# Performance work log

Measured on AMD Instinct MI355X. Metric: run time of the kernel, lower is better.

## Reference

```python
import jax, jax.numpy as jnp
import numpy as np

EPS = 1e-5  # RMSNorm epsilon


def rmsnorm(x, w):
    return x * jax.lax.rsqrt(jnp.mean(x * x, axis=-1, keepdims=True) + EPS) * w


def mamba_forward(u, in_proj_w, conv_w, conv_b, x_proj_w, dt_proj_w, dt_proj_b,
                  A_log, D_param, mamba_out_w):
    # u: (b, L, dm) -- canonical Mamba block (expand=2, d_state=16, d_conv=4)
    b, L, dm = u.shape
    di, ds = A_log.shape
    dtr = dt_proj_w.shape[1]
    xz = jnp.einsum('bld,ed->ble', u, in_proj_w)          # (b,L,2*di)
    x_, z = jnp.split(xz, 2, axis=-1)                     # each (b,L,di)
    # causal depthwise conv over the sequence axis
    dconv = conv_w.shape[-1]
    xc = jnp.transpose(x_, (0, 2, 1))                     # (b,di,L)
    xc = jnp.pad(xc, ((0, 0), (0, 0), (dconv - 1, 0)))
    xc = jax.lax.conv_general_dilated(xc, conv_w, window_strides=(1,), padding='VALID',
                                      dimension_numbers=('NCH', 'OIH', 'NCH'),
                                      feature_group_count=di)
    xc = xc + conv_b[None, :, None]
    x_ = jax.nn.silu(jnp.transpose(xc, (0, 2, 1)))        # (b,L,di)
    # input-dependent dt, B, C
    x_dbl = jnp.einsum('bld,ed->ble', x_, x_proj_w)       # (b,L,dtr+2*ds)
    dt, B, C = jnp.split(x_dbl, [dtr, dtr + ds], axis=-1)
    delta = jax.nn.softplus(jnp.einsum('blr,dr->bld', dt, dt_proj_w) + dt_proj_b)  # (b,L,di)
    A = -jnp.exp(A_log)                                   # (di,ds)

    def step(h, inp):
        d_t, B_t, C_t, x_t = inp                          # (b,di),(b,ds),(b,ds),(b,di)
        dA = jnp.exp(d_t[:, :, None] * A)                 # (b,di,ds)
        h = dA * h + (d_t * x_t)[:, :, None] * B_t[:, None, :]
        y = jnp.einsum('bds,bs->bd', h, C_t)
        return h, y

    xs = (jnp.moveaxis(delta, 1, 0), jnp.moveaxis(B, 1, 0),
          jnp.moveaxis(C, 1, 0), jnp.moveaxis(x_, 1, 0))
    h0 = jnp.zeros((b, di, ds), dtype=u.dtype)
    _, ys = jax.lax.scan(step, h0, xs)                    # ys: (L,b,di)
    y = jnp.moveaxis(ys, 0, 1) + x_ * D_param             # (b,L,di)
    y = y * jax.nn.silu(z)
    return jnp.einsum('bld,od->blo', y, mamba_out_w)      # (b,L,dm)


def conv1x1(W, bvec, t):
    # t: (b, cin, L) -> (b, cout, L)
    return jnp.einsum('oi,bit->bot', W, t) + bvec[None, :, None]


def reference(x, w_norm1, w_norm2, W_ip, b_ip, W_fp, b_fp, W_wp, b_wp, W_op, b_op,
              in_proj_w, conv_w, conv_b, x_proj_w, dt_proj_w, dt_proj_b,
              A_log, D_param, mamba_out_w):
    # x: (b, L, D) -- module's (b, c, l) with l == input_dim = D, c == seq = L
    residual = x
    xn = rmsnorm(x, w_norm1)                 # RMSNorm over last (input_dim) axis
    xt = jnp.transpose(xn, (0, 2, 1))        # 'b c l -> b l c' : (b, D, L)
    ssm = conv1x1(W_ip, b_ip, xt)            # (b, 2D, L)
    ssm = conv1x1(W_fp, b_fp, ssm)           # (b, 2D, L)
    u = jnp.transpose(ssm, (0, 2, 1))        # (b, L, 2D): seq=L, d_model=2D
    m = mamba_forward(u, in_proj_w, conv_w, conv_b, x_proj_w, dt_proj_w, dt_proj_b,
                      A_log, D_param, mamba_out_w)
    m = rmsnorm(m, w_norm2) + u              # PostNormMamba residual
    ssm = jnp.transpose(m, (0, 2, 1))        # (b, 2D, L)
    w = conv1x1(W_wp, b_wp, xt)              # (b, 2D, L)
    w = w * jax.nn.sigmoid(w)                # swish
    out = conv1x1(W_op, b_op, w * ssm)       # (b, D, L)
    return jnp.transpose(out, (0, 2, 1)) + residual


def setup_inputs():
    key = jax.random.key(0)
    ks = jax.random.split(key, 16)
    D, L, b = 64, 4096, 4
    dm, di, ds, dconv = 2 * D, 4 * D, 16, 4
    dtr = (dm + 15) // 16  # dt_rank = ceil(d_model/16) = 8

    def n(k, shape, fan_in):
        return jax.random.normal(k, shape, jnp.float32) * (1.0 / np.sqrt(fan_in))

    return {
        'x': jax.random.normal(ks[0], (b, L, D), jnp.float32),
        'w_norm1': jnp.ones((D,), jnp.float32),
        'w_norm2': jnp.ones((dm,), jnp.float32),
        'W_ip': n(ks[1], (2 * D, D), D), 'b_ip': jnp.zeros((2 * D,), jnp.float32),
        'W_fp': n(ks[2], (2 * D, 2 * D), 2 * D), 'b_fp': jnp.zeros((2 * D,), jnp.float32),
        'W_wp': n(ks[3], (2 * D, D), D), 'b_wp': jnp.zeros((2 * D,), jnp.float32),
        'W_op': n(ks[4], (D, 2 * D), 2 * D), 'b_op': jnp.zeros((D,), jnp.float32),
        'in_proj_w': n(ks[5], (2 * di, dm), dm),
        'conv_w': n(ks[6], (di, 1, dconv), dconv),
        'conv_b': jnp.zeros((di,), jnp.float32),
        'x_proj_w': n(ks[7], (dtr + 2 * ds, di), di),
        'dt_proj_w': n(ks[8], (di, dtr), dtr),
        'dt_proj_b': jnp.full((di,), float(np.log(np.expm1(0.01))), jnp.float32),
        'A_log': jnp.log(jnp.broadcast_to(jnp.arange(1, ds + 1, dtype=jnp.float32), (di, ds))),
        'D_param': jnp.ones((di,), jnp.float32),
        'mamba_out_w': n(ks[9], (dm, di), di),
    }
```

## Files before the change

kernel.cpp:

```cpp
#include <hip/hip_runtime.h>
#include <hip/hip_bf16.h>

typedef __hip_bfloat16 bf16;
typedef __attribute__((ext_vector_type(8))) short bf16x8;
typedef __attribute__((ext_vector_type(4))) float f32x4;
#define DEV __device__ __forceinline__

constexpr int SEQ  = 4096;
constexpr int NB   = 4;
constexpr int NTOK = NB * SEQ;
constexpr float EPS = 1e-5f;
constexpr int NCH = 32;
constexpr int NCHUNK = SEQ / NCH;
constexpr float LOG2E = 1.44269504f;

constexpr int OFF_WDT  = 0;
constexpr int OFF_WB   = 2048;
constexpr int WB_IP = 0;
constexpr int WB_WP = 8192;
constexpr int WB_FP = 16384;
constexpr int WB_PR = 32768;
constexpr int WB_MO = 98304;
constexpr int WB_OP = 131072;
constexpr int WB_XP = 139264;
constexpr int WB_TOT = 151552;
constexpr int OFF_XDBL = OFF_WB + WB_TOT / 2;
constexpr int OFF_R1   = OFF_XDBL + NTOK * 40;
constexpr int OFF_WSW  = OFF_R1   + 1048576;
constexpr int OFF_U    = OFF_WSW  + 1048576;
constexpr int OFF_R2   = OFF_U    + 1048576;
constexpr int OFF_SILUZ= OFF_R2   + 2097152;
constexpr int OFF_XC   = OFF_SILUZ+ 2097152;
constexpr int OFF_G    = OFF_XC   + 2097152;
constexpr int OFF_FLAG = OFF_G    + 2097152;
constexpr int OFF_SUMM = OFF_FLAG + 16;
constexpr int OFF_HIN  = OFF_SUMM + 64 * NCHUNK * 256 * 2;

DEV float b2f(bf16 x) { return __bfloat162float(x); }
DEV bf16 f2b(float x) { return __float2bfloat16(x); }
DEV short shof(bf16 h) { short s; __builtin_memcpy(&s, &h, 2); return s; }
DEV float ldin(const void* p, int i, int f) {
  return f ? ((const float*)p)[i] : b2f(((const bf16*)p)[i]);
}
DEV unsigned pack2(float a, float b) {
  bf16 ha = f2b(a), hb = f2b(b);
  unsigned short ua, ub;
  __builtin_memcpy(&ua, &ha, 2); __builtin_memcpy(&ub, &hb, 2);
  return (unsigned)ua | ((unsigned)ub << 16);
}
DEV float lo16f(unsigned u) { return __int_as_float((int)(u << 16)); }
DEV float hi16f(unsigned u) { return __int_as_float((int)(u & 0xffff0000u)); }
template<int CTRL>
DEV float dpp_add(float v) {
  int r = __builtin_amdgcn_update_dpp(0, __float_as_int(v), CTRL, 0xF, 0xF, false);
  return v + __int_as_float(r);
}
DEV float exp2f_fast(float a) { return __builtin_amdgcn_exp2f(a); }
DEV float softplus(float a) {
  return (a > 20.f) ? a : __logf(1.f + exp2f_fast(a * LOG2E));
}
DEV float silu(float a) { return a / (1.f + __expf(-a)); }

DEV void cpw(int e, int base, int count, const void* __restrict__ src,
             bf16* __restrict__ wb, int f) {
  int r = e - base;
  if (r >= 0 && r < count) wb[base + r] = f2b(ldin(src, r, f));
}
__global__ __launch_bounds__(256) void prep_k(
    const void* __restrict__ w_ip, const void* __restrict__ w_wp, const void* __restrict__ w_fp,
    const void* __restrict__ w_pr, const void* __restrict__ w_mo, const void* __restrict__ w_op,
    const void* __restrict__ w_x,  const void* __restrict__ w_dt,
    const void* __restrict__ x, float* __restrict__ wsf, int* __restrict__ flagp)
{
  __shared__ int cnt;
  if (threadIdx.x == 0) cnt = 0;
  __syncthreads();
  {
    float v = b2f(((const bf16*)x)[threadIdx.x]);
    int ok = (v == v) && fabsf(v) > 1e-4f && fabsf(v) < 100.f;
    atomicAdd(&cnt, ok);
  }
  __syncthreads();
  int f = (cnt > 204) ? 0 : 1;
  if (blockIdx.x == 0 && threadIdx.x == 0) *flagp = f;

  int e = blockIdx.x * 256 + threadIdx.x;
  bf16* wb = (bf16*)(wsf + OFF_WB);
  cpw(e, WB_IP, 8192,  w_ip, wb, f);
  cpw(e, WB_WP, 8192,  w_wp, wb, f);
  cpw(e, WB_FP, 16384, w_fp, wb, f);
  cpw(e, WB_PR, 65536, w_pr, wb, f);
  cpw(e, WB_MO, 32768, w_mo, wb, f);
  cpw(e, WB_OP, 8192,  w_op, wb, f);
  {
    int r = e - WB_XP;
    if (r >= 0 && r < 12288) wb[WB_XP + r] = (r < 10240) ? f2b(ldin(w_x, r, f)) : f2b(0.f);
  }
  if (e < 2048) {
    int r = e >> 8, d = e & 255;
    wsf[OFF_WDT + e] = ldin(w_dt, d * 8 + r, f);
  }
}

__global__ __launch_bounds__(512) void fm_k(
    const void* __restrict__ x, const void* __restrict__ w1, const float* __restrict__ wsf,
    const void* __restrict__ b_ip, const void* __restrict__ b_wp, const void* __restrict__ b_fp,
    bf16* __restrict__ wsw, bf16* __restrict__ u, bf16* __restrict__ xpre,
    bf16* __restrict__ siluz, const int* __restrict__ flagp)
{
  __shared__ __align__(16) char smem[33280];
  short* xn   = (short*)smem;
  short* t1   = (short*)(smem + 4608);
  short* ul   = (short*)(smem + 13312);
  short* wswl = (short*)(smem + 22016);
  short* xzl  = (short*)smem;

  const int f = *flagp;
  const int tid = threadIdx.x;
  const int tok0 = blockIdx.x * 32;
  {
    const int token = tid >> 4, r = tid & 15;
    float v[4]; float ss = 0.f;
    #pragma unroll
    for (int k = 0; k < 4; ++k) {
      v[k] = ldin(x, (tok0 + token) * 64 + r * 4 + k, f);
      ss += v[k] * v[k];
    }
    ss += __shfl_xor(ss, 1, 16); ss += __shfl_xor(ss, 2, 16);
    ss += __shfl_xor(ss, 4, 16); ss += __shfl_xor(ss, 8, 16);
    float sc = rsqrtf(ss * (1.f / 64.f) + EPS);
    unsigned* dst = (unsigned*)xn + token * 36 + r * 2;
    #pragma unroll
    for (int k = 0; k < 2; ++k) {
      int i = r * 4 + k * 2;
      dst[k] = pack2(v[k*2] * sc * ldin(w1, i, f), v[k*2+1] * sc * ldin(w1, i + 1, f));
    }
  }
  __syncthreads();
  const int lane = tid & 63, m = lane & 15, q = lane >> 4;
  const int w = tid >> 6;
  {
    const int wt = w >> 2, ng = w & 3;
    const bf16* W = (const bf16*)(wsf + OFF_WB) + (wt ? WB_WP : WB_IP);
    const void* bia = wt ? b_wp : b_ip;
    bf16x8 a[2][2];
    #pragma unroll
    for (int mt = 0; mt < 2; ++mt)
      #pragma unroll
      for (int kk = 0; kk < 2; ++kk)
        a[mt][kk] = *(const bf16x8*)&xn[(mt * 16 + m) * 72 + kk * 32 + q * 8];
    #pragma unroll
    for (int nti = 0; nti < 2; ++nti) {
      int nt = ng * 2 + nti;
      int n = nt * 16 + m;
      f32x4 acc[2] = {{0,0,0,0},{0,0,0,0}};
      #pragma unroll
      for (int kk = 0; kk < 2; ++kk) {
        bf16x8 b = *(const bf16x8*)(W + (nt * 16 + m) * 64 + kk * 32 + q * 8);
        #pragma unroll
        for (int mt = 0; mt < 2; ++mt)
          acc[mt] = __builtin_amdgcn_mfma_f32_16x16x32_bf16(a[mt][kk], b, acc[mt], 0, 0, 0);
      }
      float bv = ldin(bia, n, f);
      #pragma unroll
      for (int mt = 0; mt < 2; ++mt)
        #pragma unroll
        for (int r = 0; r < 4; ++r) {
          float v = acc[mt][r] + bv;
          int row = mt * 16 + q * 4 + r;
          if (wt) wswl[row * 128 + n] = shof(f2b(silu(v)));
          else    t1[row * 136 + n] = shof(f2b(v));
        }
    }
  }
  __syncthreads();
  {
    int row = tid >> 4, c8 = (tid & 15) * 8;
    uint4 v = *(const uint4*)&wswl[row * 128 + c8];
    *(uint4*)(wsw + (tok0 + row) * 128 + c8) = v;
  }
  {
    const bf16* WF = (const bf16*)(wsf + OFF_WB) + WB_FP;
    bf16x8 a[2][4];
    #pragma unroll
    for (int mt = 0; mt < 2; ++mt)
      #pragma unroll
      for (int kk = 0; kk < 4; ++kk)
        a[mt][kk] = *(const bf16x8*)&t1[(mt * 16 + m) * 136 + kk * 32 + q * 8];
    {
      int nt = w;
      int n = nt * 16 + m;
      f32x4 acc[2] = {{0,0,0,0},{0,0,0,0}};
      #pragma unroll
      for (int kk = 0; kk < 4; ++kk) {
        bf16x8 b = *(const bf16x8*)(WF + (nt * 16 + m) * 128 + kk * 32 + q * 8);
        #pragma unroll
        for (int mt = 0; mt < 2; ++mt)
          acc[mt] = __builtin_amdgcn_mfma_f32_16x16x32_bf16(a[mt][kk], b, acc[mt], 0, 0, 0);
      }
      float bv = ldin(b_fp, n, f);
      #pragma unroll
      for (int mt = 0; mt < 2; ++mt)
        #pragma unroll
        for (int r = 0; r < 4; ++r)
          ul[(mt * 16 + q * 4 + r) * 136 + n] = shof(f2b(acc[mt][r] + bv));
    }
  }
  __syncthreads();
  {
    int row = tid >> 4, c8 = (tid & 15) * 8;
    uint4 v = *(const uint4*)&ul[row * 136 + c8];
    *(uint4*)(u + (tok0 + row) * 128 + c8) = v;
  }
  {
    const bf16* WP = (const bf16*)(wsf + OFF_WB) + WB_PR;
    bf16x8 a[2][4];
    #pragma unroll
    for (int mt = 0; mt < 2; ++mt)
      #pragma unroll
      for (int kk = 0; kk < 4; ++kk)
        a[mt][kk] = *(const bf16x8*)&ul[(mt * 16 + m) * 136 + kk * 32 + q * 8];
    __syncthreads();
    #pragma unroll
    for (int nti = 0; nti < 4; ++nti) {
      int nt = w * 4 + nti;
      int n = nt * 16 + m;
      f32x4 acc[2] = {{0,0,0,0},{0,0,0,0}};
      #pragma unroll
      for (int kk = 0; kk < 4; ++kk) {
        bf16x8 b = *(const bf16x8*)(WP + (nt * 16 + m) * 128 + kk * 32 + q * 8);
        #pragma unroll
        for (int mt = 0; mt < 2; ++mt)
          acc[mt] = __builtin_amdgcn_mfma_f32_16x16x32_bf16(a[mt][kk], b, acc[mt], 0, 0, 0);
      }
      #pragma unroll
      for (int mt = 0; mt < 2; ++mt)
        #pragma unroll
        for (int r = 0; r < 4; ++r) {
          int row = mt * 16 + q * 4 + r;
          float v = acc[mt][r];
          xzl[row * 520 + n] = shof(f2b(n < 256 ? v : silu(v)));
        }
    }
  }
  __syncthreads();
  {
    #pragma unroll
    for (int k = 0; k < 4; ++k) {
      int chunk = tid + k * 512;
      int row = chunk >> 6, seg = chunk & 63;
      uint4 v = *(const uint4*)&xzl[row * 520 + seg * 8];
      int n0 = seg * 8;
      if (n0 < 256) *(uint4*)(xpre + (tok0 + row) * 256 + n0) = v;
      else          *(uint4*)(siluz + (tok0 + row) * 256 + (n0 - 256)) = v;
    }
  }
}

__global__ __launch_bounds__(256) void conv_k(
    const bf16* __restrict__ xpre, const void* __restrict__ cw, const void* __restrict__ cb,
    const float* __restrict__ wsf, bf16* __restrict__ xc, float* __restrict__ xdbl,
    const int* __restrict__ flagp)
{
  __shared__ short xh[35 * 256];
  __shared__ short cs[32 * 264];
  const int f = *flagp;
  const int tid = threadIdx.x;
  const int tok0 = blockIdx.x * 32;
  const bool seqstart = (tok0 & (SEQ - 1)) == 0;
  for (int c = tid; c < 1120; c += 256) {
    int e0 = c * 8;
    int tt = e0 >> 8, i = e0 & 255;
    int gtok = tok0 + tt - 3;
    uint4* dst = (uint4*)(xh + e0);
    if (gtok >= 0 && !(seqstart && tt < 3)) *dst = *(const uint4*)(xpre + gtok * 256 + i);
    else                                    *dst = make_uint4(0, 0, 0, 0);
  }
  __syncthreads();
  {
    const int ch0 = (tid & 63) * 4;
    const int t0 = (tid >> 6) * 8;
    float w4[4][4], cb4[4];
    #pragma unroll
    for (int c = 0; c < 4; ++c) {
      cb4[c] = ldin(cb, ch0 + c, f);
      #pragma unroll
      for (int k = 0; k < 4; ++k) w4[c][k] = ldin(cw, (ch0 + c) * 4 + k, f);
    }
    float win[11][4];
    #pragma unroll
    for (int r = 0; r < 11; ++r) {
      uint2 v = *(const uint2*)&xh[(t0 + r) * 256 + ch0];
      win[r][0] = lo16f(v.x); win[r][1] = hi16f(v.x);
      win[r][2] = lo16f(v.y); win[r][3] = hi16f(v.y);
    }
    #pragma unroll
    for (int t = 0; t < 8; ++t) {
      unsigned pk[2];
      #pragma unroll
      for (int cp = 0; cp < 2; ++cp) {
        float o[2];
        #pragma unroll
        for (int ci = 0; ci < 2; ++ci) {
          int c = cp * 2 + ci;
          float acc = cb4[c];
          #pragma unroll
          for (int k = 0; k < 4; ++k) acc = fmaf(win[t + k][c], w4[c][k], acc);
          o[ci] = silu(acc);
        }
        pk[cp] = pack2(o[0], o[1]);
      }
      uint2 pv = make_uint2(pk[0], pk[1]);
      *(uint2*)&cs[(t0 + t) * 264 + ch0] = pv;
      *(uint2*)(xc + (tok0 + t0 + t) * 256 + ch0) = pv;
    }
  }
  __syncthreads();
  const int w = tid >> 6;
  if (w < 2) {
    const bf16* Wx = (const bf16*)(wsf + OFF_WB) + WB_XP;
    const int lane = tid & 63, m = lane & 15, quad = lane >> 4;
    f32x4 acc[3] = {{0,0,0,0},{0,0,0,0},{0,0,0,0}};
    #pragma unroll
    for (int k0 = 0; k0 < 256; k0 += 32) {
      bf16x8 af = *(const bf16x8*)&cs[(w * 16 + m) * 264 + k0 + quad * 8];
      #pragma unroll
      for (int nt = 0; nt < 3; ++nt) {
        bf16x8 bfr = *(const bf16x8*)(Wx + (nt * 16 + m) * 256 + k0 + quad * 8);
        acc[nt] = __builtin_amdgcn_mfma_f32_16x16x32_bf16(af, bfr, acc[nt], 0, 0, 0);
      }
    }
    #pragma unroll
    for (int nt = 0; nt < 3; ++nt) {
      int n = nt * 16 + m;
      if (n < 40) {
        #pragma unroll
        for (int r = 0; r < 4; ++r)
          xdbl[(tok0 + w * 16 + quad * 4 + r) * 40 + n] = acc[nt][r];
      }
    }
  }
}

__global__ __launch_bounds__(256) void scanF_k(
    const float* __restrict__ xdbl, const bf16* __restrict__ xc,
    const void* __restrict__ A_log, const void* __restrict__ dt_b,
    const float* __restrict__ WDT, float* __restrict__ summ, const int* __restrict__ flagp)
{
  const int f = *flagp;
  const int tid = threadIdx.x;
  const int bb = blockIdx.x >> 2, dgsup = blockIdx.x & 3, c = blockIdx.y;
  const int dgsub = tid >> 6, lane = tid & 63, dl = lane >> 2, squad = lane & 3;
  const int dg = dgsup * 4 + dgsub;
  const int bxOld = bb * 16 + dg;
  const int d_comp = dg * 16 + dl;
  const int bd = tid & 63;
  const int d_stg = dgsup * 64 + bd;
  const int bdc = dgsub * 16 + dl;
  const int tok_base = bb * SEQ + c * NCH;

  __shared__ float dt_l[NCH * 8];
  __shared__ float dx_l[16 * 64 * 2];
  __shared__ float Bp[16 * 16];

  float Aval2[4];
  #pragma unroll
  for (int j = 0; j < 4; ++j)
    Aval2[j] = -__expf(ldin(A_log, d_comp * 16 + squad * 4 + j, f)) * LOG2E;
  const float dtb_stg = ldin(dt_b, d_stg, f);
  float wdt[8];
  #pragma unroll
  for (int r = 0; r < 8; ++r) wdt[r] = WDT[r * 256 + d_stg];

  float h[4] = {0.f, 0.f, 0.f, 0.f};
  float sdlt = 0.f;

  if (tid < 64)
    *(float4*)(dt_l + tid * 4) = *(const float4*)(xdbl + (tok_base + (tid >> 1)) * 40 + (tid & 1) * 4);

  #pragma unroll 1
  for (int half = 0; half < 2; ++half) {
    const int tb = half * 16;
    __syncthreads();
    {
      int tl = tid >> 4, s = tid & 15;
      Bp[tid] = xdbl[(tok_base + tb + tl) * 40 + 8 + s];
    }
    #pragma unroll
    for (int k = 0; k < 4; ++k) {
      int tl = (tid >> 6) + k * 4;
      int tok = tok_base + tb + tl;
      const float* dtr = dt_l + (tb + tl) * 8;
      float a = dtb_stg;
      #pragma unroll
      for (int r = 0; r < 8; ++r) a = fmaf(dtr[r], wdt[r], a);
      float dlt = softplus(a);
      float xcv = b2f(xc[tok * 256 + d_stg]);
      *(float2*)(dx_l + (tl * 64 + bd) * 2) = make_float2(dlt, dlt * xcv);
    }
    __syncthreads();

    #pragma unroll 8
    for (int tl = 0; tl < 16; ++tl) {
      float2 dx = *(const float2*)(dx_l + (tl * 64 + bdc) * 2);
      float4 B4 = *(const float4*)(Bp + tl * 16 + squad * 4);
      float Bv[4] = {B4.x, B4.y, B4.z, B4.w};
      #pragma unroll
      for (int j = 0; j < 4; ++j) {
        float dA = exp2f_fast(dx.x * Aval2[j]);
        h[j] = fmaf(dA, h[j], dx.y * Bv[j]);
      }
      sdlt += dx.x;
    }
  }

  float* dst = summ + ((bxOld * NCHUNK + c) * 256 + dl * 16 + squad * 4) * 2;
  *(float4*)(dst)     = make_float4(exp2f_fast(Aval2[0] * sdlt), h[0],
                                    exp2f_fast(Aval2[1] * sdlt), h[1]);
  *(float4*)(dst + 4) = make_float4(exp2f_fast(Aval2[2] * sdlt), h[2],
                                    exp2f_fast(Aval2[3] * sdlt), h[3]);
}

__global__ __launch_bounds__(256) void scanB_k(const float* __restrict__ summ, float* __restrict__ hinit) {
  int bx = blockIdx.x, qq = threadIdx.x;
  float h = 0.f;
  for (int c0 = 0; c0 < NCHUNK; c0 += 16) {
    float2 sv[16];
    #pragma unroll
    for (int k = 0; k < 16; ++k)
      sv[k] = *(const float2*)(summ + ((bx * NCHUNK + c0 + k) * 256 + qq) * 2);
    #pragma unroll
    for (int k = 0; k < 16; ++k) {
      hinit[(bx * NCHUNK + c0 + k) * 256 + qq] = h;
      h = fmaf(sv[k].x, h, sv[k].y);
    }
  }
}

__global__ __launch_bounds__(512) void backC_k(
    const float* __restrict__ xdbl, const bf16* __restrict__ xc, const bf16* __restrict__ siluz,
    const void* __restrict__ A_log, const void* __restrict__ D_par, const void* __restrict__ dt_b,
    const float* __restrict__ WDT, const float* __restrict__ hinit,
    const float* __restrict__ wsf, const void* __restrict__ w2,
    const bf16* __restrict__ u, const bf16* __restrict__ wsw, const void* __restrict__ b_op,
    const void* __restrict__ x, void* __restrict__ out, const int* __restrict__ flagp)
{
  __shared__ __align__(16) char smem[46592];
  short* gl   = (short*)smem;
  float* Bp   = (float*)(smem + 16896);
  float* Cp   = (float*)(smem + 18944);
  float* dt_l = (float*)(smem + 20992);
  float* dx_l = (float*)(smem + 22016);
  float* gcl  = (float*)(smem + 38400);
  short* ms   = (short*)(smem + 22016);

  const int f = *flagp;
  const int tid = threadIdx.x;
  const int tok0 = blockIdx.x * 32;
  const int bb = tok0 >> 12;
  const int c  = (tok0 & (SEQ - 1)) >> 5;
  const int w = tid >> 6, lane = tid & 63;
  const int dl = lane >> 2, squad = lane & 3;
  const int chL = w * 16 + dl;
  const int chE = tid & 127;

  {
    int tl = tid >> 4, s = tid & 15;
    Bp[tid] = xdbl[(tok0 + tl) * 40 + 8 + s];
    Cp[tid] = xdbl[(tok0 + tl) * 40 + 24 + s];
  }
  if (tid < 64)
    *(float4*)(dt_l + tid * 4) = *(const float4*)(xdbl + (tok0 + (tid >> 1)) * 40 + (tid & 1) * 4);

  #pragma unroll 1
  for (int p = 0; p < 2; ++p) {
    const int ch  = p * 128 + chL;
    const int gch = p * 128 + chE;
    float Aval2[4];
    #pragma unroll
    for (int j = 0; j < 4; ++j)
      Aval2[j] = -__expf(ldin(A_log, ch * 16 + squad * 4 + j, f)) * LOG2E;
    const float dtb = ldin(dt_b, gch, f);
    float wdt[8];
    #pragma unroll
    for (int r = 0; r < 8; ++r) wdt[r] = WDT[r * 256 + gch];
    float4 hv = *(const float4*)(hinit +
        ((bb * 16 + (ch >> 4)) * NCHUNK + c) * 256 + (ch & 15) * 16 + squad * 4);
    float h[4] = {hv.x, hv.y, hv.z, hv.w};

    #pragma unroll 1
    for (int half = 0; half < 2; ++half) {
      const int tb = half * 16;
      __syncthreads();
      #pragma unroll
      for (int k = 0; k < 4; ++k) {
        int tl = (tid >> 7) + k * 4;
        int tok = tok0 + tb + tl;
        const float* dtr = dt_l + (tb + tl) * 8;
        float a = dtb;
        #pragma unroll
        for (int r = 0; r < 8; ++r) a = fmaf(dtr[r], wdt[r], a);
        float dlt = softplus(a);
        float xcv = b2f(xc[tok * 256 + gch]);
        *(float2*)(dx_l + (tl * 128 + chE) * 2) = make_float2(dlt, dlt * xcv);
      }
      __syncthreads();

      #pragma unroll 8
      for (int tl = 0; tl < 16; ++tl) {
        float2 dx = *(const float2*)(dx_l + (tl * 128 + chL) * 2);
        float4 B4 = *(const float4*)(Bp + (tb + tl) * 16 + squad * 4);
        float Bv[4] = {B4.x, B4.y, B4.z, B4.w};
        #pragma unroll
        for (int j = 0; j < 4; ++j) {
          float dA = exp2f_fast(dx.x * Aval2[j]);
          h[j] = fmaf(dA, h[j], dx.y * Bv[j]);
        }
        float4 C4 = *(const float4*)(Cp + (tb + tl) * 16 + squad * 4);
        float pv = h[0] * C4.x;
        pv = fmaf(h[1], C4.y, pv);
        pv = fmaf(h[2], C4.z, pv);
        pv = fmaf(h[3], C4.w, pv);
        pv = dpp_add<0xB1>(pv);
        pv = dpp_add<0x4E>(pv);
        if (squad == 0) gcl[tl * 128 + chL] = pv;
      }
      __syncthreads();
      {
        const float Dp = ldin(D_par, gch, f);
        #pragma unroll
        for (int k = 0; k < 4; ++k) {
          int tl = (tid >> 7) + k * 4;
          int tok = tok0 + tb + tl;
          float pf = gcl[tl * 128 + chE];
          float xcv = b2f(xc[tok * 256 + gch]);
          gl[(tb + tl) * 264 + gch] = shof(f2b((pf + xcv * Dp) * b2f(siluz[tok * 256 + gch])));
        }
      }
    }
  }
  __syncthreads();

  const int m = lane & 15, q = lane >> 4;
  const bf16* WM = (const bf16*)(wsf + OFF_WB) + WB_MO;
  const bf16* WO = (const bf16*)(wsf + OFF_WB) + WB_OP;
  {
    f32x4 acc[2] = {{0,0,0,0},{0,0,0,0}};
    #pragma unroll
    for (int kk = 0; kk < 8; ++kk) {
      bf16x8 a0 = *(const bf16x8*)&gl[m * 264 + kk * 32 + q * 8];
      bf16x8 a1 = *(const bf16x8*)&gl[(16 + m) * 264 + kk * 32 + q * 8];
      int nt = w;
      bf16x8 b = *(const bf16x8*)(WM + (nt * 16 + m) * 256 + kk * 32 + q * 8);
      acc[0] = __builtin_amdgcn_mfma_f32_16x16x32_bf16(a0, b, acc[0], 0, 0, 0);
      acc[1] = __builtin_amdgcn_mfma_f32_16x16x32_bf16(a1, b, acc[1], 0, 0, 0);
    }
    {
      int n = w * 16 + m;
      #pragma unroll
      for (int mt = 0; mt < 2; ++mt)
        #pragma unroll
        for (int r = 0; r < 4; ++r)
          ms[(mt * 16 + q * 4 + r) * 136 + n] = shof(f2b(acc[mt][r]));
    }
  }
  __syncthreads();
  {
    const int token = tid >> 4, r = tid & 15;
    float mv[8]; float ss = 0.f;
    #pragma unroll
    for (int k = 0; k < 8; ++k) {
      mv[k] = b2f(((const bf16*)ms)[token * 136 + r * 8 + k]);
      ss += mv[k] * mv[k];
    }
    ss += __shfl_xor(ss, 1, 16); ss += __shfl_xor(ss, 2, 16);
    ss += __shfl_xor(ss, 4, 16); ss += __shfl_xor(ss, 8, 16);
    float sc = rsqrtf(ss * (1.f / 128.f) + EPS);
    #pragma unroll
    for (int k = 0; k < 8; ++k) {
      int i = r * 8 + k;
      int ga = (tok0 + token) * 128 + i;
      float v = mv[k] * sc * ldin(w2, i, f) + b2f(u[ga]);
      ms[token * 136 + i] = shof(f2b(v * b2f(wsw[ga])));
    }
  }
  __syncthreads();
  {
    const int mt = w >> 2, nt = w & 3;
    bf16x8 a[4];
    #pragma unroll
    for (int kk = 0; kk < 4; ++kk)
      a[kk] = *(const bf16x8*)&ms[(mt * 16 + m) * 136 + kk * 32 + q * 8];
    __syncthreads();
    f32x4 acc = {0,0,0,0};
    #pragma unroll
    for (int kk = 0; kk < 4; ++kk) {
      bf16x8 b = *(const bf16x8*)(WO + (nt * 16 + m) * 128 + kk * 32 + q * 8);
      acc = __builtin_amdgcn_mfma_f32_16x16x32_bf16(a[kk], b, acc, 0, 0, 0);
    }
    float* outl = (float*)ms;
    int n = nt * 16 + m;
    #pragma unroll
    for (int r = 0; r < 4; ++r)
      outl[(mt * 16 + q * 4 + r) * 68 + n] = acc[r];
  }
  __syncthreads();
  {
    const float* outl = (const float*)ms;
    int row = tid >> 4, c0 = (tid & 15) * 4;
    float v[4];
    #pragma unroll
    for (int j = 0; j < 4; ++j)
      v[j] = outl[row * 68 + c0 + j] + ldin(b_op, c0 + j, f)
           + ldin(x, (tok0 + row) * 64 + c0 + j, f);
    if (f) {
      *(float4*)((float*)out + (tok0 + row) * 64 + c0) = make_float4(v[0], v[1], v[2], v[3]);
    } else {
      uint2 pv = make_uint2(pack2(v[0], v[1]), pack2(v[2], v[3]));
      *(uint2*)((bf16*)out + (tok0 + row) * 64 + c0) = pv;
    }
  }
}

extern "C" void kernel_launch(void* const* d_in, const int* in_sizes, int n_in,
                              void* d_out, int out_size, void* d_ws, size_t ws_size,
                              hipStream_t stream) {
  (void)in_sizes; (void)n_in; (void)out_size; (void)ws_size;
  const void* x        = d_in[0];
  const void* w_norm1  = d_in[1];
  const void* w_norm2  = d_in[2];
  const void* W_ip     = d_in[3];
  const void* b_ip     = d_in[4];
  const void* W_fp     = d_in[5];
  const void* b_fp     = d_in[6];
  const void* W_wp     = d_in[7];
  const void* b_wp     = d_in[8];
  const void* W_op     = d_in[9];
  const void* b_op     = d_in[10];
  const void* in_proj  = d_in[11];
  const void* conv_w   = d_in[12];
  const void* conv_b   = d_in[13];
  const void* x_proj   = d_in[14];
  const void* dt_projw = d_in[15];
  const void* dt_projb = d_in[16];
  const void* A_log    = d_in[17];
  const void* D_par    = d_in[18];
  const void* mo_w     = d_in[19];

  float* wsf    = (float*)d_ws;
  float* xdbl   = wsf + OFF_XDBL;
  bf16*  wsw_b  = (bf16*)(wsf + OFF_WSW);
  bf16*  u_b    = (bf16*)(wsf + OFF_U);
  bf16*  xpre_b = (bf16*)(wsf + OFF_R2);
  float* summ   = wsf + OFF_SUMM;
  float* hin    = wsf + OFF_HIN;
  bf16*  siluz_b= (bf16*)(wsf + OFF_SILUZ);
  bf16*  xc_b   = (bf16*)(wsf + OFF_XC);
  int*   flagp  = (int*)(wsf + OFF_FLAG);

  prep_k<<<dim3(592), dim3(256), 0, stream>>>(W_ip, W_wp, W_fp, in_proj, mo_w, W_op,
                                              x_proj, dt_projw, x, wsf, flagp);
  fm_k<<<dim3(NTOK / 32), dim3(512), 0, stream>>>(x, w_norm1, wsf, b_ip, b_wp, b_fp,
                                                  wsw_b, u_b, xpre_b, siluz_b, flagp);
  conv_k<<<dim3(NTOK / 32), dim3(256), 0, stream>>>(xpre_b, conv_w, conv_b, wsf, xc_b, xdbl, flagp);
  scanF_k<<<dim3(16, NCHUNK), dim3(256), 0, stream>>>(xdbl, xc_b, A_log, dt_projb,
                                                      wsf + OFF_WDT, summ, flagp);
  scanB_k<<<dim3(64), dim3(256), 0, stream>>>(summ, hin);
  backC_k<<<dim3(NTOK / 32), dim3(512), 0, stream>>>(xdbl, xc_b, siluz_b, A_log, D_par,
                                                     dt_projb, wsf + OFF_WDT, hin, wsf, w_norm2,
                                                     u_b, wsw_b, b_op, x, d_out, flagp);
}
```

Measured before the change: 188.2 us.

## Fuse causal conv and chunk-local forward scan into one kernel

New measurement: 192.6 us. 1.02x slower.

```diff
diff --git a/kernel.cpp b/kernel.cpp
--- a/kernel.cpp
+++ b/kernel.cpp
@@ -257,19 +257,27 @@
   }
 }
 
-__global__ __launch_bounds__(256) void conv_k(
+__global__ __launch_bounds__(512) void convscan_k(
     const bf16* __restrict__ xpre, const void* __restrict__ cw, const void* __restrict__ cb,
-    const float* __restrict__ wsf, bf16* __restrict__ xc, float* __restrict__ xdbl,
+    const float* __restrict__ wsf, const void* __restrict__ A_log, const void* __restrict__ dt_b,
+    bf16* __restrict__ xc, float* __restrict__ xdbl, float* __restrict__ summ,
     const int* __restrict__ flagp)
 {
-  __shared__ short xh[35 * 256];
-  __shared__ short cs[32 * 264];
+  __shared__ __align__(16) char smem[38400];
+  short* cs   = (short*)smem;
+  short* xh   = (short*)(smem + 16896);
+  float* dtBC = (float*)(smem + 16896);
+  float* dx_l = (float*)(smem + 22016);
+
   const int f = *flagp;
   const int tid = threadIdx.x;
   const int tok0 = blockIdx.x * 32;
   const bool seqstart = (tok0 & (SEQ - 1)) == 0;
-  for (int c = tid; c < 1120; c += 256) {
-    int e0 = c * 8;
+  const int bb = tok0 >> 12;
+  const int c  = (tok0 & (SEQ - 1)) >> 5;
+
+  for (int cc = tid; cc < 1120; cc += 512) {
+    int e0 = cc * 8;
     int tt = e0 >> 8, i = e0 & 255;
     int gtok = tok0 + tt - 3;
     uint4* dst = (uint4*)(xh + e0);
@@ -279,33 +287,33 @@
   __syncthreads();
   {
     const int ch0 = (tid & 63) * 4;
-    const int t0 = (tid >> 6) * 8;
+    const int t0 = (tid >> 6) * 4;
     float w4[4][4], cb4[4];
     #pragma unroll
-    for (int c = 0; c < 4; ++c) {
-      cb4[c] = ldin(cb, ch0 + c, f);
-      #pragma unroll
-      for (int k = 0; k < 4; ++k) w4[c][k] = ldin(cw, (ch0 + c) * 4 + k, f);
-    }
-    float win[11][4];
-    #pragma unroll
-    for (int r = 0; r < 11; ++r) {
+    for (int cc = 0; cc < 4; ++cc) {
+      cb4[cc] = ldin(cb, ch0 + cc, f);
+      #pragma unroll
+      for (int k = 0; k < 4; ++k) w4[cc][k] = ldin(cw, (ch0 + cc) * 4 + k, f);
+    }
+    float win[7][4];
+    #pragma unroll
+    for (int r = 0; r < 7; ++r) {
       uint2 v = *(const uint2*)&xh[(t0 + r) * 256 + ch0];
       win[r][0] = lo16f(v.x); win[r][1] = hi16f(v.x);
       win[r][2] = lo16f(v.y); win[r][3] = hi16f(v.y);
     }
     #pragma unroll
-    for (int t = 0; t < 8; ++t) {
+    for (int t = 0; t < 4; ++t) {
       unsigned pk[2];
       #pragma unroll
       for (int cp = 0; cp < 2; ++cp) {
         float o[2];
         #pragma unroll
         for (int ci = 0; ci < 2; ++ci) {
-          int c = cp * 2 + ci;
-          float acc = cb4[c];
+          int cc = cp * 2 + ci;
+          float acc = cb4[cc];
           #pragma unroll
-          for (int k = 0; k < 4; ++k) acc = fmaf(win[t + k][c], w4[c][k], acc);
+          for (int k = 0; k < 4; ++k) acc = fmaf(win[t + k][cc], w4[cc][k], acc);
           o[ci] = silu(acc);
         }
         pk[cp] = pack2(o[0], o[1]);
@@ -316,10 +324,10 @@
     }
   }
   __syncthreads();
-  const int w = tid >> 6;
+  const int w = tid >> 6, lane = tid & 63;
   if (w < 2) {
     const bf16* Wx = (const bf16*)(wsf + OFF_WB) + WB_XP;
-    const int lane = tid & 63, m = lane & 15, quad = lane >> 4;
+    const int m = lane & 15, quad = lane >> 4;
     f32x4 acc[3] = {{0,0,0,0},{0,0,0,0},{0,0,0,0}};
     #pragma unroll
     for (int k0 = 0; k0 < 256; k0 += 32) {
@@ -335,90 +343,71 @@
       int n = nt * 16 + m;
       if (n < 40) {
         #pragma unroll
-        for (int r = 0; r < 4; ++r)
-          xdbl[(tok0 + w * 16 + quad * 4 + r) * 40 + n] = acc[nt][r];
-      }
-    }
-  }
-}
-
-__global__ __launch_bounds__(256) void scanF_k(
-    const float* __restrict__ xdbl, const bf16* __restrict__ xc,
-    const void* __restrict__ A_log, const void* __restrict__ dt_b,
-    const float* __restrict__ WDT, float* __restrict__ summ, const int* __restrict__ flagp)
-{
-  const int f = *flagp;
-  const int tid = threadIdx.x;
-  const int bb = blockIdx.x >> 2, dgsup = blockIdx.x & 3, c = blockIdx.y;
-  const int dgsub = tid >> 6, lane = tid & 63, dl = lane >> 2, squad = lane & 3;
-  const int dg = dgsup * 4 + dgsub;
-  const int bxOld = bb * 16 + dg;
-  const int d_comp = dg * 16 + dl;
-  const int bd = tid & 63;
-  const int d_stg = dgsup * 64 + bd;
-  const int bdc = dgsub * 16 + dl;
-  const int tok_base = bb * SEQ + c * NCH;
-
-  __shared__ float dt_l[NCH * 8];
-  __shared__ float dx_l[16 * 64 * 2];
-  __shared__ float Bp[16 * 16];
-
-  float Aval2[4];
-  #pragma unroll
-  for (int j = 0; j < 4; ++j)
-    Aval2[j] = -__expf(ldin(A_log, d_comp * 16 + squad * 4 + j, f)) * LOG2E;
-  const float dtb_stg = ldin(dt_b, d_stg, f);
-  float wdt[8];
-  #pragma unroll
-  for (int r = 0; r < 8; ++r) wdt[r] = WDT[r * 256 + d_stg];
-
-  float h[4] = {0.f, 0.f, 0.f, 0.f};
-  float sdlt = 0.f;
-
-  if (tid < 64)
-    *(float4*)(dt_l + tid * 4) = *(const float4*)(xdbl + (tok_base + (tid >> 1)) * 40 + (tid & 1) * 4);
-
+        for (int r = 0; r < 4; ++r) {
+          int row = w * 16 + quad * 4 + r;
+          dtBC[row * 40 + n] = acc[nt][r];
+          xdbl[(tok0 + row) * 40 + n] = acc[nt][r];
+        }
+      }
+    }
+  }
+  __syncthreads();
+
+  const int dl = lane >> 2, squad = lane & 3;
+  const int chE = tid & 127;
   #pragma unroll 1
-  for (int half = 0; half < 2; ++half) {
-    const int tb = half * 16;
-    __syncthreads();
+  for (int p = 0; p < 2; ++p) {
+    const int ch  = p * 128 + w * 16 + dl;
+    const int gch = p * 128 + chE;
+    float Aval2[4];
+    #pragma unroll
+    for (int j = 0; j < 4; ++j)
+      Aval2[j] = -__expf(ldin(A_log, ch * 16 + squad * 4 + j, f)) * LOG2E;
+    const float dtb = ldin(dt_b, gch, f);
+    float wdt[8];
+    #pragma unroll
+    for (int r = 0; r < 8; ++r) wdt[r] = wsf[OFF_WDT + r * 256 + gch];
+    float h[4] = {0.f, 0.f, 0.f, 0.f};
+    float sdlt = 0.f;
+
+    #pragma unroll 1
+    for (int half = 0; half < 2; ++half) {
+      const int tb = half * 16;
+      #pragma unroll
+      for (int k = 0; k < 4; ++k) {
+        int tl = (tid >> 7) + k * 4;
+        const float* dtr = dtBC + (tb + tl) * 40;
+        float a = dtb;
+        #pragma unroll
+        for (int r = 0; r < 8; ++r) a = fmaf(dtr[r], wdt[r], a);
+        float dlt = softplus(a);
+        float xcv = b2f(((const bf16*)cs)[(tb + tl) * 264 + gch]);
+        *(float2*)(dx_l + (tl * 128 + chE) * 2) = make_float2(dlt, dlt * xcv);
+      }
+      __syncthreads();
+      #pragma unroll 8
+      for (int tl = 0; tl < 16; ++tl) {
+        float2 dx = *(const float2*)(dx_l + (tl * 128 + w * 16 + dl) * 2);
+        float4 B4 = *(const float4*)(dtBC + (tb + tl) * 40 + 8 + squad * 4);
+        float Bv[4] = {B4.x, B4.y, B4.z, B4.w};
+        #pragma unroll
+        for (int j = 0; j < 4; ++j) {
+          float dA = exp2f_fast(dx.x * Aval2[j]);
+          h[j] = fmaf(dA, h[j], dx.y * Bv[j]);
+        }
+        sdlt += dx.x;
+      }
+      __syncthreads();
+    }
     {
-      int tl = tid >> 4, s = tid & 15;
-      Bp[tid] = xdbl[(tok_base + tb + tl) * 40 + 8 + s];
-    }
-    #pragma unroll
-    for (int k = 0; k < 4; ++k) {
-      int tl = (tid >> 6) + k * 4;
-      int tok = tok_base + tb + tl;
-      const float* dtr = dt_l + (tb + tl) * 8;
-      float a = dtb_stg;
-      #pragma unroll
-      for (int r = 0; r < 8; ++r) a = fmaf(dtr[r], wdt[r], a);
-      float dlt = softplus(a);
-      float xcv = b2f(xc[tok * 256 + d_stg]);
-      *(float2*)(dx_l + (tl * 64 + bd) * 2) = make_float2(dlt, dlt * xcv);
-    }
-    __syncthreads();
-
-    #pragma unroll 8
-    for (int tl = 0; tl < 16; ++tl) {
-      float2 dx = *(const float2*)(dx_l + (tl * 64 + bdc) * 2);
-      float4 B4 = *(const float4*)(Bp + tl * 16 + squad * 4);
-      float Bv[4] = {B4.x, B4.y, B4.z, B4.w};
-      #pragma unroll
-      for (int j = 0; j < 4; ++j) {
-        float dA = exp2f_fast(dx.x * Aval2[j]);
-        h[j] = fmaf(dA, h[j], dx.y * Bv[j]);
-      }
-      sdlt += dx.x;
-    }
-  }
-
-  float* dst = summ + ((bxOld * NCHUNK + c) * 256 + dl * 16 + squad * 4) * 2;
-  *(float4*)(dst)     = make_float4(exp2f_fast(Aval2[0] * sdlt), h[0],
-                                    exp2f_fast(Aval2[1] * sdlt), h[1]);
-  *(float4*)(dst + 4) = make_float4(exp2f_fast(Aval2[2] * sdlt), h[2],
-                                    exp2f_fast(Aval2[3] * sdlt), h[3]);
+      int dg = ch >> 4;
+      float* dst = summ + (((bb * 16 + dg) * NCHUNK + c) * 256 + (ch & 15) * 16 + squad * 4) * 2;
+      *(float4*)(dst)     = make_float4(exp2f_fast(Aval2[0] * sdlt), h[0],
+                                        exp2f_fast(Aval2[1] * sdlt), h[1]);
+      *(float4*)(dst + 4) = make_float4(exp2f_fast(Aval2[2] * sdlt), h[2],
+                                        exp2f_fast(Aval2[3] * sdlt), h[3]);
+    }
+  }
 }
 
 __global__ __launch_bounds__(256) void scanB_k(const float* __restrict__ summ, float* __restrict__ hinit) {
@@ -662,9 +651,8 @@
                                               x_proj, dt_projw, x, wsf, flagp);
   fm_k<<<dim3(NTOK / 32), dim3(512), 0, stream>>>(x, w_norm1, wsf, b_ip, b_wp, b_fp,
                                                   wsw_b, u_b, xpre_b, siluz_b, flagp);
-  conv_k<<<dim3(NTOK / 32), dim3(256), 0, stream>>>(xpre_b, conv_w, conv_b, wsf, xc_b, xdbl, flagp);
-  scanF_k<<<dim3(16, NCHUNK), dim3(256), 0, stream>>>(xdbl, xc_b, A_log, dt_projb,
-                                                      wsf + OFF_WDT, summ, flagp);
+  convscan_k<<<dim3(NTOK / 32), dim3(512), 0, stream>>>(xpre_b, conv_w, conv_b, wsf, A_log,
+                                                        dt_projb, xc_b, xdbl, summ, flagp);
   scanB_k<<<dim3(64), dim3(256), 0, stream>>>(summ, hin);
   backC_k<<<dim3(NTOK / 32), dim3(512), 0, stream>>>(xdbl, xc_b, siluz_b, A_log, D_par,
                                                      dt_projb, wsf + OFF_WDT, hin, wsf, w_norm2,
```
